# Kernel optimization log

Hardware: AMD Instinct MI355X
Metric: run time of the kernel (lower is better)

The kernel has to match this reference:

```python
import jax, jax.numpy as jnp
import numpy as np

B, N = 2, 4096
BN_EPS = 1e-5
INV_STD = np.float32(1.0 / np.sqrt(1.0 + BN_EPS))  # BN inference: running_mean=0, running_var=1


def pconv(x, w):
    # 1x1 Conv1d == per-point matmul: x [B,C,N], w [Cout,Cin] -> [B,Cout,N]
    return jnp.einsum('oc,bcn->bon', w, x)


def bn(x, g, b):
    # inference BatchNorm1d with mean=0, var=1
    return x * (INV_STD * g)[None, :, None] + b[None, :, None]


def sa_layer(x, qk_w, v_w, v_b, t_w, t_b, g, b):
    # PCT offset-attention. q_conv and k_conv share weights, so energy is a Gram matrix.
    xq = pconv(x, qk_w)                                   # [B, C//2, N]
    energy = jnp.einsum('bcn,bcm->bnm', xq, xq)           # [B, N, N]
    att = jax.nn.softmax(energy, axis=-1)
    att = att / (1e-9 + att.sum(axis=1, keepdims=True))   # extra L1 renorm over dim=1
    xv = pconv(x, v_w) + v_b[None, :, None]               # [B, C, N]
    x_r = jnp.einsum('bcn,bnm->bcm', xv, att)             # [B, C, N]
    # offset=True branch
    x_r = jax.nn.relu(bn(pconv(x - x_r, t_w) + t_b[None, :, None], g, b))
    return x + x_r


def _forward(x, conv1_w, bn1_g, bn1_b, conv2_w, bn2_g, bn2_b, conv3_w, bn3_g, bn3_b,
             pt1_w, pt1_g, pt1_b, pt2_w, pt2_g, pt2_b,
             sa1_qk, sa1_vw, sa1_vb, sa1_tw, sa1_tb, sa1_g, sa1_b,
             sa2_qk, sa2_vw, sa2_vb, sa2_tw, sa2_tb, sa2_g, sa2_b,
             cf_w, cf_g, cf_b, s1_w, s1_g, s1_b, s2_w, s2_g, s2_b, s3_w):
    h = jnp.transpose(x, (0, 2, 1))                       # [B, 3, N]
    h = jax.nn.relu(bn(pconv(h, conv1_w), bn1_g, bn1_b))  # [B, 64, N]
    h = jax.nn.relu(bn(pconv(h, conv2_w), bn2_g, bn2_b))  # [B, 128, N]
    h = jax.nn.relu(bn(pconv(h, conv3_w), bn3_g, bn3_b))  # [B, 256, N]
    # Point_Transformer_Last
    h = jax.nn.relu(bn(pconv(h, pt1_w), pt1_g, pt1_b))
    h = jax.nn.relu(bn(pconv(h, pt2_w), pt2_g, pt2_b))
    x1 = sa_layer(h, sa1_qk, sa1_vw, sa1_vb, sa1_tw, sa1_tb, sa1_g, sa1_b)
    x2 = sa_layer(x1, sa2_qk, sa2_vw, sa2_vb, sa2_tw, sa2_tb, sa2_g, sa2_b)
    # original forward reuses sa2's weights for layers 3 and 4
    x3 = sa_layer(x2, sa2_qk, sa2_vw, sa2_vb, sa2_tw, sa2_tb, sa2_g, sa2_b)
    x4 = sa_layer(x3, sa2_qk, sa2_vw, sa2_vb, sa2_tw, sa2_tb, sa2_g, sa2_b)
    h = jnp.concatenate([x1, x2, x3, x4], axis=1)         # [B, 1024, N]
    face = jax.nn.leaky_relu(bn(pconv(h, cf_w), cf_g, cf_b), 0.2)  # [B, 512, N]
    gmax = jnp.max(face, axis=2, keepdims=True)           # adaptive_max_pool1d(.,1)
    h = jnp.concatenate([face, jnp.broadcast_to(gmax, face.shape)], axis=1)  # [B, 1024, N]
    h = jax.nn.leaky_relu(bn(pconv(h, s1_w), s1_g, s1_b), 0.2)
    h = jax.nn.leaky_relu(bn(pconv(h, s2_w), s2_g, s2_b), 0.2)
    h = pconv(h, s3_w)                                    # [B, 50, N]
    return jnp.transpose(h, (0, 2, 1))                    # [B, N, 50]


def setup_inputs() -> dict:
    key = jax.random.key(0)
    kit = iter(jax.random.split(key, 80))
    def W(co, ci):
        return jax.random.normal(next(kit), (co, ci), dtype=jnp.float32) / np.float32(np.sqrt(ci))
    def G(c):
        return 1.0 + 0.1 * jax.random.normal(next(kit), (c,), dtype=jnp.float32)
    def Bv(c):
        return 0.1 * jax.random.normal(next(kit), (c,), dtype=jnp.float32)
    d = {}
    d['x'] = jax.random.normal(next(kit), (B, N, 3), dtype=jnp.float32)
    d['conv1_w'] = W(64, 3);   d['bn1_g'] = G(64);  d['bn1_b'] = Bv(64)
    d['conv2_w'] = W(128, 64); d['bn2_g'] = G(128); d['bn2_b'] = Bv(128)
    d['conv3_w'] = W(256, 128); d['bn3_g'] = G(256); d['bn3_b'] = Bv(256)
    d['pt1_w'] = W(256, 256); d['pt1_g'] = G(256); d['pt1_b'] = Bv(256)
    d['pt2_w'] = W(256, 256); d['pt2_g'] = G(256); d['pt2_b'] = Bv(256)
    for p in ('sa1', 'sa2'):
        d[p + '_qk'] = 0.1 * W(128, 256)  # small scale keeps softmax unsaturated
        d[p + '_vw'] = W(256, 256); d[p + '_vb'] = Bv(256)
        d[p + '_tw'] = W(256, 256); d[p + '_tb'] = Bv(256)
        d[p + '_g'] = G(256); d[p + '_b'] = Bv(256)
    d['cf_w'] = W(512, 1024); d['cf_g'] = G(512); d['cf_b'] = Bv(512)
    d['s1_w'] = W(512, 1024); d['s1_g'] = G(512); d['s1_b'] = Bv(512)
    d['s2_w'] = W(256, 512); d['s2_g'] = G(256); d['s2_b'] = Bv(256)
    d['s3_w'] = W(50, 256)
    return d


def reference(x, conv1_w, bn1_g, bn1_b, conv2_w, bn2_g, bn2_b, conv3_w, bn3_g, bn3_b,
              pt1_w, pt1_g, pt1_b, pt2_w, pt2_g, pt2_b,
              sa1_qk, sa1_vw, sa1_vb, sa1_tw, sa1_tb, sa1_g, sa1_b,
              sa2_qk, sa2_vw, sa2_vb, sa2_tw, sa2_tb, sa2_g, sa2_b,
              cf_w, cf_g, cf_b, s1_w, s1_g, s1_b, s2_w, s2_g, s2_b, s3_w):
    return _forward(x, conv1_w, bn1_g, bn1_b, conv2_w, bn2_g, bn2_b, conv3_w, bn3_g, bn3_b,
                    pt1_w, pt1_g, pt1_b, pt2_w, pt2_g, pt2_b,
                    sa1_qk, sa1_vw, sa1_vb, sa1_tw, sa1_tb, sa1_g, sa1_b,
                    sa2_qk, sa2_vw, sa2_vb, sa2_tw, sa2_tb, sa2_g, sa2_b,
                    cf_w, cf_g, cf_b, s1_w, s1_g, s1_b, s2_w, s2_g, s2_b, s3_w)
```

## Files before the change

kernel.cpp:

```cpp
#include <hip/hip_runtime.h>
#include <hip/hip_bf16.h>


#define NPTS 4096
#define BATCH 2
#define MSPLIT 4
#define RSSPLIT 8
static constexpr float INV_STD = 0.9999950000374997f;

__device__ __forceinline__ float bf2f(unsigned short u) {
    return __uint_as_float(((unsigned int)u) << 16);
}
__device__ __forceinline__ unsigned short f2bf(float f) {
    unsigned int x = __float_as_uint(f);
    unsigned int r = (x + 0x7FFFu + ((x >> 16) & 1u)) >> 16;
    return (unsigned short)r;
}

__device__ __forceinline__ void async16(const unsigned short* g, unsigned short* l)
{
    __builtin_amdgcn_global_load_lds(
        (const __attribute__((address_space(1))) unsigned int*)(const void*)g,
        (__attribute__((address_space(3))) unsigned int*)(void*)l,
        16, 0, 0);
}

typedef __attribute__((ext_vector_type(8))) short short8;
typedef __attribute__((ext_vector_type(4))) float f32x4;

struct WSplit {
    const float* src[14];
    int n[14];
    long long off[14];
};

__global__ __launch_bounds__(256)
void presplit_k(WSplit d, unsigned short* __restrict__ wbuf)
{
    int wi = blockIdx.y;
    int i = blockIdx.x * 256 + threadIdx.x;
    int n = d.n[wi];
    if (i >= n) return;
    float v = d.src[wi][i];
    unsigned short h = f2bf(v);
    unsigned short* dst = wbuf + d.off[wi];
    dst[i] = h;
    dst[n + i] = f2bf(v - bf2f(h));
}

__device__ __forceinline__ void nt_epilogue(
    float y, int rg, int cg, int b, int Nb,
    const float* bias, int bias_mode,
    const float* bng, const float* bnb,
    const unsigned short* res, long long res_bs, int res_ld, long long res_po,
    int act, int out_mode,
    void* Cp, long long c_bs, int c_ld, long long c_po)
{
    if (bias) {
        if (bias_mode == 3)      y += bias[rg];
        else if (bias_mode == 2) y += bias[b * Nb + cg];
        else                     y += bias[cg];
    }
    if (bng) y = y * (INV_STD * bng[cg]) + bnb[cg];
    if (act == 1) y = fmaxf(y, 0.f);
    else if (act == 2) y = (y > 0.f) ? y : 0.2f * y;
    if (res) {
        long long ri_ = (long long)b * res_bs + (long long)rg * res_ld + cg;
        y += bf2f(res[ri_]) + bf2f(res[res_po + ri_]);
    }
    long long ci = (long long)b * c_bs + (long long)rg * c_ld + cg;
    if (out_mode == 0) {
        unsigned short* C = (unsigned short*)Cp;
        unsigned short h = f2bf(y);
        C[ci] = h;
        C[c_po + ci] = f2bf(y - bf2f(h));
    } else if (out_mode == 1) {
        ((unsigned short*)Cp)[ci] = f2bf(y);
    } else {
        if (cg < Nb) ((float*)Cp)[ci] = y;
    }
}

__global__ __launch_bounds__(256)
void gemm_nt_split(const unsigned short* __restrict__ A, long long a_bs, int a_lda, long long a_po,
                   const unsigned short* __restrict__ B, long long b_bs, int b_lda, long long b_po,
                   void* __restrict__ Cp, long long c_bs, int c_ld, long long c_po,
                   int Nb, int K,
                   const float* __restrict__ bias, int bias_mode,
                   const float* __restrict__ bng, const float* __restrict__ bnb,
                   const unsigned short* __restrict__ res, long long res_bs, int res_ld, long long res_po,
                   int act, int out_mode)
{
    __shared__ unsigned short As[2][64 * 64];
    __shared__ unsigned short Bs[2][64 * 64];
    const int b = blockIdx.z;
    const int m0 = blockIdx.y * 64, n0 = blockIdx.x * 64;
    const int t = threadIdx.x;
    const int lane = t & 63, w = t >> 6;
    const int wr = (w >> 1) * 32, wc = (w & 1) * 32;
    const int ml = lane & 15, q = lane >> 4;

    f32x4 acc[2][2] = {};

    for (int k0 = 0; k0 < K; k0 += 64) {
        __syncthreads();
        #pragma unroll
        for (int e = 0; e < 2; e++) {
            int idx = t + e * 256;
            int row = idx >> 3, blk = idx & 7;
            int gblk = blk ^ (row & 7);
            int lofs = (e * 256 + (t & 192)) * 8;
            const unsigned short* sA = A + (long long)b * a_bs
                                     + (long long)(m0 + row) * a_lda + k0 + gblk * 8;
            const unsigned short* sB = B + (long long)b * b_bs
                                     + (long long)(n0 + row) * b_lda + k0 + gblk * 8;
            async16(sA,        &As[0][0] + lofs);
            async16(sA + a_po, &As[1][0] + lofs);
            async16(sB,        &Bs[0][0] + lofs);
            async16(sB + b_po, &Bs[1][0] + lofs);
        }
        __syncthreads();
        #pragma unroll
        for (int kk = 0; kk < 2; kk++) {
            short8 ah[2], al[2], bh[2], bl[2];
            #pragma unroll
            for (int it = 0; it < 2; it++) {
                int row = wr + it * 16 + ml;
                int slot = (kk * 4 + q) ^ (row & 7);
                ah[it] = *(const short8*)(&As[0][row * 64 + slot * 8]);
                al[it] = *(const short8*)(&As[1][row * 64 + slot * 8]);
            }
            #pragma unroll
            for (int jt = 0; jt < 2; jt++) {
                int row = wc + jt * 16 + ml;
                int slot = (kk * 4 + q) ^ (row & 7);
                bh[jt] = *(const short8*)(&Bs[0][row * 64 + slot * 8]);
                bl[jt] = *(const short8*)(&Bs[1][row * 64 + slot * 8]);
            }
            #pragma unroll
            for (int it = 0; it < 2; it++)
                #pragma unroll
                for (int jt = 0; jt < 2; jt++) {
                    acc[it][jt] = __builtin_amdgcn_mfma_f32_16x16x32_bf16(ah[it], bh[jt], acc[it][jt], 0, 0, 0);
                    acc[it][jt] = __builtin_amdgcn_mfma_f32_16x16x32_bf16(ah[it], bl[jt], acc[it][jt], 0, 0, 0);
                    acc[it][jt] = __builtin_amdgcn_mfma_f32_16x16x32_bf16(al[it], bh[jt], acc[it][jt], 0, 0, 0);
                }
        }
    }

    #pragma unroll
    for (int it = 0; it < 2; it++)
        #pragma unroll
        for (int jt = 0; jt < 2; jt++)
            #pragma unroll
            for (int r = 0; r < 4; r++)
                nt_epilogue(acc[it][jt][r], m0 + wr + it * 16 + q * 4 + r,
                            n0 + wc + jt * 16 + ml, b, Nb,
                            bias, bias_mode, bng, bnb, res, res_bs, res_ld, res_po,
                            act, out_mode, Cp, c_bs, c_ld, c_po);
}

__global__ __launch_bounds__(256)
void gemm_nt_splitB(const unsigned short* __restrict__ A, long long a_bs, int a_lda, long long a_po,
                    const unsigned short* __restrict__ B, long long b_bs, int b_lda, long long b_po,
                    void* __restrict__ Cp, long long c_bs, int c_ld, long long c_po,
                    int Nb, int K,
                    const float* __restrict__ bias, int bias_mode,
                    const float* __restrict__ bng, const float* __restrict__ bnb,
                    const unsigned short* __restrict__ res, long long res_bs, int res_ld, long long res_po,
                    int act, int out_mode)
{
    __shared__ unsigned short As[2][2][64 * 64];
    __shared__ unsigned short Bs[2][2][64 * 64];
    const int b = blockIdx.z;
    const int m0 = blockIdx.y * 64, n0 = blockIdx.x * 64;
    const int t = threadIdx.x;
    const int lane = t & 63, w = t >> 6;
    const int wr = (w >> 1) * 32, wc = (w & 1) * 32;
    const int ml = lane & 15, q = lane >> 4;

    f32x4 acc[2][2] = {};

    for (int k0 = 0; k0 < K; k0 += 128) {
        __syncthreads();
        #pragma unroll
        for (int sub = 0; sub < 2; sub++) {
            int kb = k0 + sub * 64;
            #pragma unroll
            for (int e = 0; e < 2; e++) {
                int idx = t + e * 256;
                int row = idx >> 3, blk = idx & 7;
                int gblk = blk ^ (row & 7);
                int lofs = (e * 256 + (t & 192)) * 8;
                const unsigned short* sA = A + (long long)b * a_bs
                                         + (long long)(m0 + row) * a_lda + kb + gblk * 8;
                const unsigned short* sB = B + (long long)b * b_bs
                                         + (long long)(n0 + row) * b_lda + kb + gblk * 8;
                async16(sA,        &As[0][sub][0] + lofs);
                async16(sA + a_po, &As[1][sub][0] + lofs);
                async16(sB,        &Bs[0][sub][0] + lofs);
                async16(sB + b_po, &Bs[1][sub][0] + lofs);
            }
        }
        __syncthreads();
        #pragma unroll
        for (int sub = 0; sub < 2; sub++)
            #pragma unroll
            for (int kk = 0; kk < 2; kk++) {
                short8 ah[2], al[2], bh[2], bl[2];
                #pragma unroll
                for (int it = 0; it < 2; it++) {
                    int row = wr + it * 16 + ml;
                    int slot = (kk * 4 + q) ^ (row & 7);
                    ah[it] = *(const short8*)(&As[0][sub][row * 64 + slot * 8]);
                    al[it] = *(const short8*)(&As[1][sub][row * 64 + slot * 8]);
                }
                #pragma unroll
                for (int jt = 0; jt < 2; jt++) {
                    int row = wc + jt * 16 + ml;
                    int slot = (kk * 4 + q) ^ (row & 7);
                    bh[jt] = *(const short8*)(&Bs[0][sub][row * 64 + slot * 8]);
                    bl[jt] = *(const short8*)(&Bs[1][sub][row * 64 + slot * 8]);
                }
                #pragma unroll
                for (int it = 0; it < 2; it++)
                    #pragma unroll
                    for (int jt = 0; jt < 2; jt++) {
                        acc[it][jt] = __builtin_amdgcn_mfma_f32_16x16x32_bf16(ah[it], bh[jt], acc[it][jt], 0, 0, 0);
                        acc[it][jt] = __builtin_amdgcn_mfma_f32_16x16x32_bf16(ah[it], bl[jt], acc[it][jt], 0, 0, 0);
                        acc[it][jt] = __builtin_amdgcn_mfma_f32_16x16x32_bf16(al[it], bh[jt], acc[it][jt], 0, 0, 0);
                    }
            }
    }

    #pragma unroll
    for (int it = 0; it < 2; it++)
        #pragma unroll
        for (int jt = 0; jt < 2; jt++)
            #pragma unroll
            for (int r = 0; r < 4; r++)
                nt_epilogue(acc[it][jt][r], m0 + wr + it * 16 + q * 4 + r,
                            n0 + wc + jt * 16 + ml, b, Nb,
                            bias, bias_mode, bng, bnb, res, res_bs, res_ld, res_po,
                            act, out_mode, Cp, c_bs, c_ld, c_po);
}

__global__ __launch_bounds__(256)
void rs_k(const unsigned short* __restrict__ xq, float* __restrict__ rs)
{
    __shared__ unsigned short Kq[2][2][64 * 64];
    const int b = blockIdx.z;
    const int p0 = blockIdx.y * 64;
    const int m_beg = blockIdx.x * (NPTS / RSSPLIT);
    const unsigned short* xqB = xq + (long long)b * NPTS * 128;
    const int t = threadIdx.x;
    const int lane = t & 63, w = t >> 6;
    const int pw = w * 16;
    const int ml = lane & 15, q = lane >> 4;

    short8 af[4];
    #pragma unroll
    for (int ks = 0; ks < 4; ks++)
        af[ks] = *(const short8*)(xqB + (long long)(p0 + pw + ml) * 128 + ks * 32 + q * 8);

    float rsum[4] = {0.f, 0.f, 0.f, 0.f};

    auto stageK = [&](int m0, int buf) {
        #pragma unroll
        for (int e = 0; e < 4; e++) {
            int idx = t + e * 256;
            int sub = idx >> 9, row = (idx >> 3) & 63, blk = idx & 7;
            int gblk = blk ^ (row & 7);
            int lofs = (e * 256 + (t & 192)) * 8;
            async16(xqB + (long long)(m0 + row) * 128 + sub * 64 + gblk * 8,
                    &Kq[buf][0][0] + lofs);
        }
    };

    constexpr int NIT = (NPTS / RSSPLIT) / 64;
    stageK(m_beg, 0);
    __syncthreads();

    for (int it = 0; it < NIT; ++it) {
        const int m0 = m_beg + it * 64;
        const int cur = it & 1;
        if (it + 1 < NIT) stageK(m0 + 64, cur ^ 1);
        f32x4 acc[4] = {};
        #pragma unroll
        for (int ks = 0; ks < 4; ks++) {
            int kh = ks >> 1, kk = ks & 1;
            #pragma unroll
            for (int jt = 0; jt < 4; jt++) {
                int row = jt * 16 + ml;
                int slot = (kk * 4 + q) ^ (row & 7);
                short8 bf = *(const short8*)(&Kq[cur][kh][row * 64 + slot * 8]);
                acc[jt] = __builtin_amdgcn_mfma_f32_16x16x32_bf16(af[ks], bf, acc[jt], 0, 0, 0);
            }
        }
        #pragma unroll
        for (int jt = 0; jt < 4; jt++)
            #pragma unroll
            for (int r = 0; r < 4; r++)
                rsum[r] += __expf(acc[jt][r]);
        __syncthreads();
    }
    #pragma unroll
    for (int r = 0; r < 4; r++) {
        float s = rsum[r];
        s += __shfl_xor(s, 1); s += __shfl_xor(s, 2);
        s += __shfl_xor(s, 4); s += __shfl_xor(s, 8);
        if (ml == 0) atomicAdd(&rs[b * NPTS + p0 + pw + q * 4 + r], s);
    }
}

__global__ __launch_bounds__(256)
void attn_pv(const unsigned short* __restrict__ xq,
             const unsigned short* __restrict__ xv,
             const float* __restrict__ rs,
             float* __restrict__ part,
             float* __restrict__ csp)
{
    __shared__ unsigned short Kq[2][2][64 * 64];
    __shared__ unsigned short Pl[2][64][72];
    const int z = blockIdx.z, b = z / MSPLIT, ms = z % MSPLIT;
    const int p0 = blockIdx.y * 64;
    const unsigned short* xqB = xq + (long long)b * NPTS * 128;
    const unsigned short* xvB = xv + (long long)b * 256 * NPTS;
    const float* rsB = rs + b * NPTS;
    const int t = threadIdx.x;
    const int lane = t & 63, w = t >> 6;
    const int pw = w * 16;
    const int cw = w * 64;
    const int ml = lane & 15, q = lane >> 4;

    short8 af[4];
    #pragma unroll
    for (int ks = 0; ks < 4; ks++)
        af[ks] = *(const short8*)(xqB + (long long)(p0 + pw + ml) * 128 + ks * 32 + q * 8);

    f32x4 pv[4][4] = {};
    float csr[4] = {0.f, 0.f, 0.f, 0.f};

    auto stageK = [&](int m0, int buf) {
        #pragma unroll
        for (int e = 0; e < 4; e++) {
            int idx = t + e * 256;
            int sub = idx >> 9, row = (idx >> 3) & 63, blk = idx & 7;
            int gblk = blk ^ (row & 7);
            int lofs = (e * 256 + (t & 192)) * 8;
            async16(xqB + (long long)(m0 + row) * 128 + sub * 64 + gblk * 8,
                    &Kq[buf][0][0] + lofs);
        }
    };

    const int m_beg = ms * (NPTS / MSPLIT);
    constexpr int NIT = (NPTS / MSPLIT) / 64;
    stageK(m_beg, 0);
    __syncthreads();

    for (int it = 0; it < NIT; ++it) {
        const int m0 = m_beg + it * 64;
        const int cur = it & 1;
        if (it + 1 < NIT) stageK(m0 + 64, cur ^ 1);
        short8 bv[2][4];
        #pragma unroll
        for (int kk = 0; kk < 2; kk++)
            #pragma unroll
            for (int jt = 0; jt < 4; jt++) {
                int row = cw + jt * 16 + ml;
                bv[kk][jt] = *(const short8*)(xvB + (long long)row * NPTS
                                              + m0 + kk * 32 + q * 8);
            }
        f32x4 acc[4] = {};
        #pragma unroll
        for (int ks = 0; ks < 4; ks++) {
            int kh = ks >> 1, kk = ks & 1;
            #pragma unroll
            for (int jt = 0; jt < 4; jt++) {
                int row = jt * 16 + ml;
                int slot = (kk * 4 + q) ^ (row & 7);
                short8 bf = *(const short8*)(&Kq[cur][kh][row * 64 + slot * 8]);
                acc[jt] = __builtin_amdgcn_mfma_f32_16x16x32_bf16(af[ks], bf, acc[jt], 0, 0, 0);
            }
        }
        #pragma unroll
        for (int jt = 0; jt < 4; jt++) {
            float rvm = 1.f / rsB[m0 + jt * 16 + ml];
            #pragma unroll
            for (int r = 0; r < 4; r++) {
                float pvv = __expf(acc[jt][r]) * rvm;
                csr[r] += pvv;
                Pl[cur][pw + q * 4 + r][jt * 16 + ml] = f2bf(pvv);
            }
        }
        __syncthreads();
        #pragma unroll
        for (int kk = 0; kk < 2; kk++) {
            short8 ap[4];
            #pragma unroll
            for (int pst = 0; pst < 4; pst++)
                ap[pst] = *(const short8*)(&Pl[cur][pst * 16 + ml][kk * 32 + q * 8]);
            #pragma unroll
            for (int jt = 0; jt < 4; jt++)
                #pragma unroll
                for (int pst = 0; pst < 4; pst++)
                    pv[pst][jt] = __builtin_amdgcn_mfma_f32_16x16x32_bf16(
                        ap[pst], bv[kk][jt], pv[pst][jt], 0, 0, 0);
        }
    }
    #pragma unroll
    for (int r = 0; r < 4; r++) {
        float s = csr[r];
        s += __shfl_xor(s, 1); s += __shfl_xor(s, 2);
        s += __shfl_xor(s, 4); s += __shfl_xor(s, 8);
        if (ml == 0) csp[(long long)z * NPTS + p0 + pw + q * 4 + r] = s;
    }
    float* C = part + (long long)z * ((long long)NPTS * 256);
    #pragma unroll
    for (int pst = 0; pst < 4; pst++)
        #pragma unroll
        for (int jt = 0; jt < 4; jt++)
            #pragma unroll
            for (int r = 0; r < 4; r++) {
                int rg = p0 + pst * 16 + q * 4 + r;
                int cg = cw + jt * 16 + ml;
                C[(long long)rg * 256 + cg] = pv[pst][jt][r];
            }
}

__global__ __launch_bounds__(256)
void conv1_k(const float* __restrict__ x, const float* __restrict__ w,
             const float* __restrict__ g, const float* __restrict__ bb,
             unsigned short* __restrict__ h, long long h_po)
{
    int b = blockIdx.y;
    int p = blockIdx.x * 4 + (threadIdx.x >> 6);
    int c = threadIdx.x & 63;
    const float* xp = x + ((long long)b * NPTS + p) * 3;
    float y = xp[0] * w[c * 3] + xp[1] * w[c * 3 + 1] + xp[2] * w[c * 3 + 2];
    y = y * (INV_STD * g[c]) + bb[c];
    y = fmaxf(y, 0.f);
    long long i = ((long long)b * NPTS + p) * 64 + c;
    unsigned short hi = f2bf(y);
    h[i] = hi;
    h[h_po + i] = f2bf(y - bf2f(hi));
}

__global__ __launch_bounds__(256)
void zero_k(float* __restrict__ p, int n)
{
    int i = blockIdx.x * 256 + threadIdx.x;
    if (i < n) p[i] = 0.f;
}

__global__ __launch_bounds__(256)
void diff_k(const unsigned short* __restrict__ xin, long long x_bs, int x_ld, long long x_po,
            const float* __restrict__ part, const float* __restrict__ csp,
            unsigned short* __restrict__ d, long long d_po)
{
    long long i = (long long)blockIdx.x * 256 + threadIdx.x;
    int b = blockIdx.y;
    int p = (int)(i >> 8), c = (int)(i & 255);
    long long xi = (long long)b * x_bs + (long long)p * x_ld + c;
    float xv = bf2f(xin[xi]) + bf2f(xin[x_po + xi]);
    float xr = 0.f, den = 1e-9f;
    #pragma unroll
    for (int ks = 0; ks < MSPLIT; ks++) {
        int z = b * MSPLIT + ks;
        xr  += part[(long long)z * ((long long)NPTS * 256) + i];
        den += csp[(long long)z * NPTS + p];
    }
    float v = xv - xr / den;
    long long di = (long long)b * NPTS * 256 + i;
    unsigned short hi = f2bf(v);
    d[di] = hi;
    d[d_po + di] = f2bf(v - bf2f(hi));
}

__global__ __launch_bounds__(256)
void gmaxp_k(const unsigned short* __restrict__ face, long long f_po, float* __restrict__ pm)
{
    int c = blockIdx.x * 256 + threadIdx.x;
    int ch = blockIdx.y;
    int b = blockIdx.z;
    float m = -3.4e38f;
    for (int j = 0; j < 256; j++) {
        long long i = ((long long)b * NPTS + ch * 256 + j) * 512 + c;
        m = fmaxf(m, bf2f(face[i]) + bf2f(face[f_po + i]));
    }
    pm[((long long)b * 16 + ch) * 512 + c] = m;
}

__global__ __launch_bounds__(256)
void gmaxr_k(const float* __restrict__ pm, float* __restrict__ gm)
{
    int idx = blockIdx.x * 256 + threadIdx.x;
    int b = idx >> 9, c = idx & 511;
    float m = -3.4e38f;
    for (int ch = 0; ch < 16; ch++)
        m = fmaxf(m, pm[((long long)b * 16 + ch) * 512 + c]);
    gm[idx] = m;
}

__global__ __launch_bounds__(256)
void bias2_k(const float* __restrict__ w, const float* __restrict__ g, float* __restrict__ b2)
{
    int o = blockIdx.x * 256 + threadIdx.x;
    int b = blockIdx.y;
    if (o >= 512) return;
    float s = 0.f;
    for (int c = 0; c < 512; c++) s += w[(long long)o * 1024 + 512 + c] * g[b * 512 + c];
    b2[b * 512 + o] = s;
}

extern "C" void kernel_launch(void* const* d_in, const int* in_sizes, int n_in,
                              void* d_out, int out_size, void* d_ws, size_t ws_size,
                              hipStream_t stream)
{
    const float* x       = (const float*)d_in[0];
    const float* conv1_w = (const float*)d_in[1];
    const float* bn1_g   = (const float*)d_in[2];
    const float* bn1_b   = (const float*)d_in[3];
    const float* conv2_w = (const float*)d_in[4];
    const float* bn2_g   = (const float*)d_in[5];
    const float* bn2_b   = (const float*)d_in[6];
    const float* conv3_w = (const float*)d_in[7];
    const float* bn3_g   = (const float*)d_in[8];
    const float* bn3_b   = (const float*)d_in[9];
    const float* pt1_w   = (const float*)d_in[10];
    const float* pt1_g   = (const float*)d_in[11];
    const float* pt1_b   = (const float*)d_in[12];
    const float* pt2_w   = (const float*)d_in[13];
    const float* pt2_g   = (const float*)d_in[14];
    const float* pt2_b   = (const float*)d_in[15];
    const float* sa_qk[2] = {(const float*)d_in[16], (const float*)d_in[23]};
    const float* sa_vw[2] = {(const float*)d_in[17], (const float*)d_in[24]};
    const float* sa_vb[2] = {(const float*)d_in[18], (const float*)d_in[25]};
    const float* sa_tw[2] = {(const float*)d_in[19], (const float*)d_in[26]};
    const float* sa_tb[2] = {(const float*)d_in[20], (const float*)d_in[27]};
    const float* sa_g[2]  = {(const float*)d_in[21], (const float*)d_in[28]};
    const float* sa_b[2]  = {(const float*)d_in[22], (const float*)d_in[29]};
    const float* cf_w = (const float*)d_in[30];
    const float* cf_g = (const float*)d_in[31];
    const float* cf_b = (const float*)d_in[32];
    const float* s1_w = (const float*)d_in[33];
    const float* s1_g = (const float*)d_in[34];
    const float* s1_b = (const float*)d_in[35];
    const float* s2_w = (const float*)d_in[36];
    const float* s2_g = (const float*)d_in[37];
    const float* s2_b = (const float*)d_in[38];
    const float* s3_w = (const float*)d_in[39];

    char* base = (char*)d_ws;
    size_t off = 0;
    auto alloc = [&](size_t bytes) -> void* {
        void* p = base + off;
        off = (off + bytes + 255) & ~(size_t)255;
        return p;
    };
    const long long N = NPTS;
    const long long PO64   = (long long)BATCH * N * 64;
    const long long PO128  = (long long)BATCH * N * 128;
    const long long PO256  = (long long)BATCH * N * 256;
    const long long PO512  = (long long)BATCH * N * 512;
    const long long PO1024 = (long long)BATCH * N * 1024;

    unsigned short* S1  = (unsigned short*)alloc(2 * PO256 * 2);
    unsigned short* S2  = (unsigned short*)alloc(2 * PO256 * 2);
    unsigned short* Dv  = (unsigned short*)alloc(2 * PO256 * 2);
    unsigned short* cat = (unsigned short*)alloc(2 * PO1024 * 2);
    unsigned short* face = (unsigned short*)alloc(2 * PO512 * 2);
    unsigned short* xq  = (unsigned short*)alloc((size_t)BATCH * N * 128 * 2);
    unsigned short* xv  = (unsigned short*)alloc((size_t)BATCH * 256 * N * 2);
    unsigned short* s1b = (unsigned short*)alloc(2 * PO512 * 2);
    unsigned short* s2b = (unsigned short*)alloc(2 * PO256 * 2);
    float* part = (float*)alloc((size_t)BATCH * MSPLIT * N * 256 * 4);
    float* csp  = (float*)alloc((size_t)BATCH * MSPLIT * N * 4);
    float* rs = (float*)alloc((size_t)BATCH * N * 4);
    float* pm = (float*)alloc((size_t)BATCH * 16 * 512 * 4);
    float* gm = (float*)alloc((size_t)BATCH * 512 * 4);
    float* b2 = (float*)alloc((size_t)BATCH * 512 * 4);
    unsigned short* wb = (unsigned short*)alloc((size_t)3400000 * 2);

    WSplit wd;
    const float* wsrc[14] = {conv2_w, conv3_w, pt1_w, pt2_w, sa_qk[0], sa_qk[1],
                             sa_vw[0], sa_vw[1], sa_tw[0], sa_tw[1], cf_w, s1_w, s2_w, s3_w};
    int wn[14] = {128*64, 256*128, 256*256, 256*256, 128*256, 128*256,
                  256*256, 256*256, 256*256, 256*256, 512*1024, 512*1024, 256*512, 50*256};
    long long wo[14]; long long acc_ = 0;
    for (int i = 0; i < 14; i++) { wd.src[i] = wsrc[i]; wd.n[i] = wn[i]; wd.off[i] = acc_; wo[i] = acc_; acc_ += 2LL * wn[i]; }
    presplit_k<<<dim3((512*1024 + 255) / 256, 14), 256, 0, stream>>>(wd, wb);
    auto W = [&](int i) { return wb + wo[i]; };

    auto nt = [&](const unsigned short* A, long long a_bs, int a_lda, long long a_po,
                  const unsigned short* B, long long b_bs, int b_lda, long long b_po,
                  void* C, long long c_bs, int c_ld, long long c_po,
                  int Mrows, int Nb, int K,
                  const float* bias, int bias_mode,
                  const float* bng, const float* bnb,
                  const unsigned short* res, long long res_bs, int res_ld, long long res_po,
                  int act, int out_mode) {
        dim3 g((Nb + 63) / 64, Mrows / 64, BATCH);
        gemm_nt_split<<<g, 256, 0, stream>>>(A, a_bs, a_lda, a_po, B, b_bs, b_lda, b_po,
                                             C, c_bs, c_ld, c_po, Nb, K,
                                             bias, bias_mode, bng, bnb,
                                             res, res_bs, res_ld, res_po, act, out_mode);
    };
    auto ntB = [&](const unsigned short* A, long long a_bs, int a_lda, long long a_po,
                   const unsigned short* B, long long b_bs, int b_lda, long long b_po,
                   void* C, long long c_bs, int c_ld, long long c_po,
                   int Mrows, int Nb, int K,
                   const float* bias, int bias_mode,
                   const float* bng, const float* bnb,
                   const unsigned short* res, long long res_bs, int res_ld, long long res_po,
                   int act, int out_mode) {
        dim3 g((Nb + 63) / 64, Mrows / 64, BATCH);
        gemm_nt_splitB<<<g, 256, 0, stream>>>(A, a_bs, a_lda, a_po, B, b_bs, b_lda, b_po,
                                              C, c_bs, c_ld, c_po, Nb, K,
                                              bias, bias_mode, bng, bnb,
                                              res, res_bs, res_ld, res_po, act, out_mode);
    };

    conv1_k<<<dim3(NPTS / 4, BATCH), 256, 0, stream>>>(x, conv1_w, bn1_g, bn1_b, S1, PO64);
    nt(S1, N * 64, 64, PO64,    W(0), 0, 64, wn[0],  S2, N * 128, 128, PO128,
       NPTS, 128, 64,  nullptr, 0, bn2_g, bn2_b, nullptr, 0, 0, 0, 1, 0);
    ntB(S2, N * 128, 128, PO128, W(1), 0, 128, wn[1], S1, N * 256, 256, PO256,
        NPTS, 256, 128, nullptr, 0, bn3_g, bn3_b, nullptr, 0, 0, 0, 1, 0);
    ntB(S1, N * 256, 256, PO256, W(2), 0, 256, wn[2], S2, N * 256, 256, PO256,
        NPTS, 256, 256, nullptr, 0, pt1_g, pt1_b, nullptr, 0, 0, 0, 1, 0);
    ntB(S2, N * 256, 256, PO256, W(3), 0, 256, wn[3], S1, N * 256, 256, PO256,
        NPTS, 256, 256, nullptr, 0, pt2_g, pt2_b, nullptr, 0, 0, 0, 1, 0);

    for (int i = 0; i < 4; i++) {
        int p = (i == 0) ? 0 : 1;
        const unsigned short* xin = (i == 0) ? S1 : cat + (size_t)(i - 1) * 256;
        long long xin_bs = (i == 0) ? N * 256 : N * 1024;
        int xin_ld = (i == 0) ? 256 : 1024;
        long long xin_po = (i == 0) ? PO256 : PO1024;

        ntB(xin, xin_bs, xin_ld, xin_po, W(4 + p), 0, 256, wn[4 + p],
            xq, N * 128, 128, 0, NPTS, 128, 256,
            nullptr, 0, nullptr, nullptr, nullptr, 0, 0, 0, 0, 1);
        ntB(W(6 + p), 0, 256, wn[6 + p], xin, xin_bs, xin_ld, xin_po,
            xv, 256 * N, NPTS, 0, 256, NPTS, 256,
            sa_vb[p], 3, nullptr, nullptr, nullptr, 0, 0, 0, 0, 1);
        zero_k<<<(BATCH * NPTS + 255) / 256, 256, 0, stream>>>(rs, BATCH * NPTS);
        rs_k<<<dim3(RSSPLIT, NPTS / 64, BATCH), 256, 0, stream>>>(xq, rs);
        attn_pv<<<dim3(1, NPTS / 64, BATCH * MSPLIT), 256, 0, stream>>>(
            xq, xv, rs, part, csp);
        diff_k<<<dim3(NPTS * 256 / 256, BATCH), 256, 0, stream>>>(
            xin, xin_bs, xin_ld, xin_po, part, csp, Dv, PO256);
        ntB(Dv, N * 256, 256, PO256, W(8 + p), 0, 256, wn[8 + p],
            cat + (size_t)i * 256, N * 1024, 1024, PO1024,
            NPTS, 256, 256, sa_tb[p], 1, sa_g[p], sa_b[p],
            xin, xin_bs, xin_ld, xin_po, 1, 0);
    }

    nt(cat, N * 1024, 1024, PO1024, W(10), 0, 1024, wn[10],
       face, N * 512, 512, PO512, NPTS, 512, 1024,
       nullptr, 0, cf_g, cf_b, nullptr, 0, 0, 0, 2, 0);
    gmaxp_k<<<dim3(2, 16, BATCH), 256, 0, stream>>>(face, PO512, pm);
    gmaxr_k<<<dim3(BATCH * 512 / 256), 256, 0, stream>>>(pm, gm);
    bias2_k<<<dim3(2, BATCH), 256, 0, stream>>>(s1_w, gm, b2);
    nt(face, N * 512, 512, PO512, W(11), 0, 1024, wn[11],
       s1b, N * 512, 512, PO512, NPTS, 512, 512,
       b2, 2, s1_g, s1_b, nullptr, 0, 0, 0, 2, 0);
    ntB(s1b, N * 512, 512, PO512, W(12), 0, 512, wn[12],
        s2b, N * 256, 256, PO256, NPTS, 256, 512,
        nullptr, 0, s2_g, s2_b, nullptr, 0, 0, 0, 2, 0);
    ntB(s2b, N * 256, 256, PO256, W(13), 0, 256, wn[13],
        d_out, N * 50, 50, 0, NPTS, 50, 256,
        nullptr, 0, nullptr, nullptr, nullptr, 0, 0, 0, 0, 2);
}
```

Measured before the change: 792.7 us.

## Split attn_pv output channels across two blocks and single-buffer LDS

Adds a channel-split grid dimension to the attention P·V kernel so each block computes 128 of the 256 value channels, doubling block count and halving accumulator registers. The score matmul and exp are now recomputed redundantly in both channel blocks. LDS staging drops from double to single buffering, with the next K tile prefetch issued after the P tile barrier, which reduces LDS footprint but gives less load/compute overlap. Only the first channel block writes column sums.

```diff
diff --git a/kernel.cpp b/kernel.cpp
--- a/kernel.cpp
+++ b/kernel.cpp
@@ -5,6 +5,7 @@
 #define NPTS 4096
 #define BATCH 2
 #define MSPLIT 4
+#define CSPLIT 2
 #define RSSPLIT 8
 static constexpr float INV_STD = 0.9999950000374997f;
 
@@ -320,17 +321,19 @@
              float* __restrict__ part,
              float* __restrict__ csp)
 {
-    __shared__ unsigned short Kq[2][2][64 * 64];
-    __shared__ unsigned short Pl[2][64][72];
+    __shared__ unsigned short Kq[2][64 * 64];
+    __shared__ unsigned short Pl[64][72];
     const int z = blockIdx.z, b = z / MSPLIT, ms = z % MSPLIT;
+    const int cs = blockIdx.x;
     const int p0 = blockIdx.y * 64;
+    const int cb = cs * 128;
     const unsigned short* xqB = xq + (long long)b * NPTS * 128;
     const unsigned short* xvB = xv + (long long)b * 256 * NPTS;
     const float* rsB = rs + b * NPTS;
     const int t = threadIdx.x;
     const int lane = t & 63, w = t >> 6;
     const int pw = w * 16;
-    const int cw = w * 64;
+    const int cw = w * 32;
     const int ml = lane & 15, q = lane >> 4;
 
     short8 af[4];
@@ -338,10 +341,10 @@
     for (int ks = 0; ks < 4; ks++)
         af[ks] = *(const short8*)(xqB + (long long)(p0 + pw + ml) * 128 + ks * 32 + q * 8);
 
-    f32x4 pv[4][4] = {};
+    f32x4 pv[4][2] = {};
     float csr[4] = {0.f, 0.f, 0.f, 0.f};
 
-    auto stageK = [&](int m0, int buf) {
+    auto stageK = [&](int m0) {
         #pragma unroll
         for (int e = 0; e < 4; e++) {
             int idx = t + e * 256;
@@ -349,25 +352,23 @@
             int gblk = blk ^ (row & 7);
             int lofs = (e * 256 + (t & 192)) * 8;
             async16(xqB + (long long)(m0 + row) * 128 + sub * 64 + gblk * 8,
-                    &Kq[buf][0][0] + lofs);
+                    &Kq[0][0] + lofs);
         }
     };
 
     const int m_beg = ms * (NPTS / MSPLIT);
     constexpr int NIT = (NPTS / MSPLIT) / 64;
-    stageK(m_beg, 0);
-    __syncthreads();
+    stageK(m_beg);
 
     for (int it = 0; it < NIT; ++it) {
         const int m0 = m_beg + it * 64;
-        const int cur = it & 1;
-        if (it + 1 < NIT) stageK(m0 + 64, cur ^ 1);
-        short8 bv[2][4];
+        __syncthreads();
+        short8 bv[2][2];
         #pragma unroll
         for (int kk = 0; kk < 2; kk++)
             #pragma unroll
-            for (int jt = 0; jt < 4; jt++) {
-                int row = cw + jt * 16 + ml;
+            for (int jt = 0; jt < 2; jt++) {
+                int row = cb + cw + jt * 16 + ml;
                 bv[kk][jt] = *(const short8*)(xvB + (long long)row * NPTS
                                               + m0 + kk * 32 + q * 8);
             }
@@ -379,7 +380,7 @@
             for (int jt = 0; jt < 4; jt++) {
                 int row = jt * 16 + ml;
                 int slot = (kk * 4 + q) ^ (row & 7);
-                short8 bf = *(const short8*)(&Kq[cur][kh][row * 64 + slot * 8]);
+                short8 bf = *(const short8*)(&Kq[kh][row * 64 + slot * 8]);
                 acc[jt] = __builtin_amdgcn_mfma_f32_16x16x32_bf16(af[ks], bf, acc[jt], 0, 0, 0);
             }
         }
@@ -390,40 +391,43 @@
             for (int r = 0; r < 4; r++) {
                 float pvv = __expf(acc[jt][r]) * rvm;
                 csr[r] += pvv;
-                Pl[cur][pw + q * 4 + r][jt * 16 + ml] = f2bf(pvv);
+                Pl[pw + q * 4 + r][jt * 16 + ml] = f2bf(pvv);
             }
         }
         __syncthreads();
+        if (it + 1 < NIT) stageK(m0 + 64);
         #pragma unroll
         for (int kk = 0; kk < 2; kk++) {
             short8 ap[4];
             #pragma unroll
             for (int pst = 0; pst < 4; pst++)
-                ap[pst] = *(const short8*)(&Pl[cur][pst * 16 + ml][kk * 32 + q * 8]);
-            #pragma unroll
-            for (int jt = 0; jt < 4; jt++)
+                ap[pst] = *(const short8*)(&Pl[pst * 16 + ml][kk * 32 + q * 8]);
+            #pragma unroll
+            for (int jt = 0; jt < 2; jt++)
                 #pragma unroll
                 for (int pst = 0; pst < 4; pst++)
                     pv[pst][jt] = __builtin_amdgcn_mfma_f32_16x16x32_bf16(
                         ap[pst], bv[kk][jt], pv[pst][jt], 0, 0, 0);
         }
     }
-    #pragma unroll
-    for (int r = 0; r < 4; r++) {
-        float s = csr[r];
-        s += __shfl_xor(s, 1); s += __shfl_xor(s, 2);
-        s += __shfl_xor(s, 4); s += __shfl_xor(s, 8);
-        if (ml == 0) csp[(long long)z * NPTS + p0 + pw + q * 4 + r] = s;
+    if (cs == 0) {
+        #pragma unroll
+        for (int r = 0; r < 4; r++) {
+            float s = csr[r];
+            s += __shfl_xor(s, 1); s += __shfl_xor(s, 2);
+            s += __shfl_xor(s, 4); s += __shfl_xor(s, 8);
+            if (ml == 0) csp[(long long)z * NPTS + p0 + pw + q * 4 + r] = s;
+        }
     }
     float* C = part + (long long)z * ((long long)NPTS * 256);
     #pragma unroll
     for (int pst = 0; pst < 4; pst++)
         #pragma unroll
-        for (int jt = 0; jt < 4; jt++)
+        for (int jt = 0; jt < 2; jt++)
             #pragma unroll
             for (int r = 0; r < 4; r++) {
                 int rg = p0 + pst * 16 + q * 4 + r;
-                int cg = cw + jt * 16 + ml;
+                int cg = cb + cw + jt * 16 + ml;
                 C[(long long)rg * 256 + cg] = pv[pst][jt][r];
             }
 }
@@ -646,7 +650,7 @@
             sa_vb[p], 3, nullptr, nullptr, nullptr, 0, 0, 0, 0, 1);
         zero_k<<<(BATCH * NPTS + 255) / 256, 256, 0, stream>>>(rs, BATCH * NPTS);
         rs_k<<<dim3(RSSPLIT, NPTS / 64, BATCH), 256, 0, stream>>>(xq, rs);
-        attn_pv<<<dim3(1, NPTS / 64, BATCH * MSPLIT), 256, 0, stream>>>(
+        attn_pv<<<dim3(CSPLIT, NPTS / 64, BATCH * MSPLIT), 256, 0, stream>>>(
             xq, xv, rs, part, csp);
         diff_k<<<dim3(NPTS * 256 / 256, BATCH), 256, 0, stream>>>(
             xin, xin_bs, xin_ld, xin_po, part, csp, Dv, PO256);
```

Result: slower. 890.8 us (+12.4%).
